# Kernel optimization log

Hardware: AMD Instinct MI355X
Metric: run time of the kernel (lower is better)

## Reference

```python
import jax, jax.numpy as jnp
import numpy as np
from jax.ops import segment_sum

N_NODES = 50000
N_EDGES = 800000
IN_DIM, HID_DIM, OUT_DIM = 128, 256, 128


def _glorot(key, shape):
    lim = np.sqrt(6.0 / (shape[0] + shape[1]))
    return jax.random.uniform(key, shape, jnp.float32, -lim, lim)


def setup_inputs() -> dict:
    key = jax.random.key(0)
    ks = jax.random.split(key, 4)
    x = jax.random.normal(ks[0], (N_NODES, IN_DIM), jnp.float32)
    edge_index = jax.random.randint(ks[1], (2, N_EDGES), 0, N_NODES, jnp.int64)
    W1 = _glorot(ks[2], (IN_DIM, HID_DIM))
    b1 = jnp.zeros((HID_DIM,), jnp.float32)
    W2 = _glorot(ks[3], (HID_DIM, OUT_DIM))
    b2 = jnp.zeros((OUT_DIM,), jnp.float32)
    return {"x": x, "edge_index": edge_index, "W1": W1, "b1": b1, "W2": W2, "b2": b2}


def gcn_conv(x, W, b, src, dst, n_nodes):
    # PyG GCNConv: x' = D^{-1/2} (A + I) D^{-1/2} (x W) + b
    h = x @ W  # [N, F_out]
    deg = segment_sum(jnp.ones_like(src, dtype=h.dtype), dst, num_segments=n_nodes) + 1.0  # +1 self loop
    dinv = jax.lax.rsqrt(deg)  # [N]
    norm = dinv[src] * dinv[dst]  # per-edge norm [E]
    msg = h[src] * norm[:, None]  # [E, F_out]
    agg = segment_sum(msg, dst, num_segments=n_nodes)
    agg = agg + h * (dinv * dinv)[:, None]  # self-loop term: norm_ii = dinv_i^2
    return agg + b


def reference(x, edge_index, W1, b1, W2, b2):
    src, dst = edge_index[0], edge_index[1]
    h = gcn_conv(x, W1, b1, src, dst, N_NODES)
    h = jax.nn.relu(h)
    out = gcn_conv(h, W2, b2, src, dst, N_NODES)
    return out
```

## Files before the change

kernel.cpp:

```cpp
#include <hip/hip_runtime.h>

#define N_NODES 50000
#define N_EDGES 800000
#define IN_DIM  128
#define HID_DIM 256
#define OUT_DIM 128
#define BUCKET_CAP 64
#define NCOARSE 196
#define CHUNK 4000
#define NBLK1 200
#define SEGCAP 64
#define HLD 264

typedef __attribute__((ext_vector_type(8))) short short8;
typedef __attribute__((ext_vector_type(4))) float f32x4;

__device__ inline ushort f2b(float f) {
    union { float f; unsigned u; } v; v.f = f;
    return (ushort)((v.u + 0x7FFFu + ((v.u >> 16) & 1u)) >> 16);
}
__device__ inline float b2f(ushort h) {
    union { unsigned u; float f; } v; v.u = ((unsigned)h) << 16;
    return v.f;
}
__device__ inline float2 u2f2(unsigned u) {
    float2 r; r.x = b2f((ushort)(u & 0xFFFFu)); r.y = b2f((ushort)(u >> 16)); return r;
}
__device__ inline unsigned f2u2(float a, float b) {
    return (unsigned)f2b(a) | ((unsigned)f2b(b) << 16);
}
__device__ inline void fma8(float2* acc, uint4 u, float n) {
    float2 v0 = u2f2(u.x), v1 = u2f2(u.y), v2 = u2f2(u.z), v3 = u2f2(u.w);
    acc[0].x += v0.x * n; acc[0].y += v0.y * n;
    acc[1].x += v1.x * n; acc[1].y += v1.y * n;
    acc[2].x += v2.x * n; acc[2].y += v2.y * n;
    acc[3].x += v3.x * n; acc[3].y += v3.y * n;
}


__global__ __launch_bounds__(256) void prep_kernel(const float* __restrict__ x,
                                                   const float* __restrict__ W1,
                                                   const float* __restrict__ W2,
                                                   const int* __restrict__ src,
                                                   const int* __restrict__ dst,
                                                   ushort* __restrict__ xb,
                                                   ushort* __restrict__ w1t,
                                                   ushort* __restrict__ w2t,
                                                   int* __restrict__ bcnt,
                                                   int* __restrict__ binbuf) {
    __shared__ int vals[CHUNK];
    __shared__ ushort lpos[CHUNK];
    __shared__ unsigned char lbin[CHUNK];
    __shared__ int hist[NCOARSE];
    const int b = blockIdx.x;
    const int t = threadIdx.x;
    if (b < 6250) {
        int i = b * 256 + t;
        float4 v = ((const float4*)x)[i];
        ushort4 o; o.x = f2b(v.x); o.y = f2b(v.y); o.z = f2b(v.z); o.w = f2b(v.w);
        ((ushort4*)xb)[i] = o;
    } else if (b < 6506) {
        int i = (b - 6250) * 256 + t;
        if (i < 32768) {
            int n = i >> 7, k = i & 127;
            w1t[i] = f2b(W1[k * HID_DIM + n]);
        } else {
            int j = i - 32768;
            int n = j >> 8, k = j & 255;
            w2t[j] = f2b(W2[k * OUT_DIM + n]);
        }
    } else {
        const int blk = b - 6506;
        const int e0 = blk * CHUNK;
        for (int i = t; i < NCOARSE; i += 256) hist[i] = 0;
        __syncthreads();
        for (int i = t; i < CHUNK; i += 256) {
            int s = src[e0 + i], d = dst[e0 + i];
            int bin = d >> 8;
            vals[i] = (s << 8) | (d & 255);
            lbin[i] = (unsigned char)bin;
            lpos[i] = (ushort)atomicAdd(&hist[bin], 1);
        }
        __syncthreads();
        for (int i = t; i < NCOARSE; i += 256) {
            int h = hist[i]; if (h > SEGCAP) h = SEGCAP;
            bcnt[i * NBLK1 + blk] = h;
        }
        for (int i = t; i < CHUNK; i += 256) {
            int bin = lbin[i];
            int p = lpos[i];
            if (p < SEGCAP) binbuf[((size_t)bin * NBLK1 + blk) * SEGCAP + p] = vals[i];
        }
    }
}


__global__ __launch_bounds__(256) void binpass2_kernel(const int* __restrict__ bcnt,
                                                       const int* __restrict__ binbuf,
                                                       int* __restrict__ cnt,
                                                       float* __restrict__ dinv,
                                                       int* __restrict__ bucket) {
    __shared__ int lcnt[256];
    __shared__ int lm[NBLK1];
    __shared__ int lbuck[256 * BUCKET_CAP];
    const int bin = blockIdx.x;
    const int t = threadIdx.x;
    lcnt[t] = 0;
    if (t < NBLK1) lm[t] = bcnt[bin * NBLK1 + t];
    __syncthreads();
    const int* bb = binbuf + (size_t)bin * NBLK1 * SEGCAP;
    for (int f = t; f < NBLK1 * SEGCAP; f += 256) {
        int blk = f >> 6;
        int sl = f & 63;
        if (sl < lm[blk]) {
            int v = bb[f];
            int dl = v & 255;
            int pos = atomicAdd(&lcnt[dl], 1);
            if (pos < BUCKET_CAP) lbuck[dl * BUCKET_CAP + pos] = v >> 8;
        }
    }
    __syncthreads();
    const int node0 = bin * 256;
    int node = node0 + t;
    if (node < N_NODES) {
        int c = lcnt[t] > BUCKET_CAP ? BUCKET_CAP : lcnt[t];
        cnt[node] = c;
        dinv[node] = rsqrtf((float)c + 1.0f);
    }
    int nvalid = N_NODES - node0; if (nvalid > 256) nvalid = 256;
    if (nvalid <= 0) return;
    int total4 = (nvalid * BUCKET_CAP) >> 2;
    int4* d4 = (int4*)(bucket + (size_t)node0 * BUCKET_CAP);
    const int4* s4 = (const int4*)lbuck;
    for (int j = t; j < total4; j += 256) d4[j] = s4[j];
}


__global__ __launch_bounds__(256) void gather0_kernel(const int* __restrict__ cnt,
                                                      const int* __restrict__ bucket,
                                                      const float* __restrict__ dinv,
                                                      const ushort* __restrict__ xb,
                                                      ushort* __restrict__ aggxb) {
    const int w = blockIdx.x * 4 + (threadIdx.x >> 6);
    const int lane = threadIdx.x & 63;
    const int grp = lane >> 4, sub = lane & 15;
    const int n = cnt[w];
    const float dd = dinv[w];
    int sv = 0; float nv = 0.f;
    if (lane < n) { sv = bucket[w * BUCKET_CAP + lane]; nv = dinv[sv] * dd; }

    float2 acc[4];
    if (grp == 0) {
        uint4 su = ((const uint4*)(xb + (size_t)w * IN_DIM))[sub];
        float sd = dd * dd;
        acc[0] = u2f2(su.x); acc[1] = u2f2(su.y); acc[2] = u2f2(su.z); acc[3] = u2f2(su.w);
#pragma unroll
        for (int j = 0; j < 4; ++j) { acc[j].x *= sd; acc[j].y *= sd; }
    } else {
#pragma unroll
        for (int j = 0; j < 4; ++j) acc[j] = {0.f, 0.f};
    }

    const int nr = (n + 15) & ~15;
    for (int i = 0; i < nr; i += 16) {
        int s0 = __shfl(sv, i + grp),      s1 = __shfl(sv, i + 4 + grp);
        int s2 = __shfl(sv, i + 8 + grp),  s3 = __shfl(sv, i + 12 + grp);
        float n0 = __shfl(nv, i + grp),     n1 = __shfl(nv, i + 4 + grp);
        float n2 = __shfl(nv, i + 8 + grp), n3 = __shfl(nv, i + 12 + grp);
        uint4 u0 = ((const uint4*)(xb + (size_t)s0 * IN_DIM))[sub];
        uint4 u1 = ((const uint4*)(xb + (size_t)s1 * IN_DIM))[sub];
        uint4 u2 = ((const uint4*)(xb + (size_t)s2 * IN_DIM))[sub];
        uint4 u3 = ((const uint4*)(xb + (size_t)s3 * IN_DIM))[sub];
        fma8(acc, u0, n0); fma8(acc, u1, n1); fma8(acc, u2, n2); fma8(acc, u3, n3);
    }
#pragma unroll
    for (int j = 0; j < 4; ++j) {
        acc[j].x += __shfl_down(acc[j].x, 32); acc[j].y += __shfl_down(acc[j].y, 32);
        acc[j].x += __shfl_down(acc[j].x, 16); acc[j].y += __shfl_down(acc[j].y, 16);
    }
    if (lane < 16) {
        uint4 o = {f2u2(acc[0].x, acc[0].y), f2u2(acc[1].x, acc[1].y),
                   f2u2(acc[2].x, acc[2].y), f2u2(acc[3].x, acc[3].y)};
        ((uint4*)(aggxb + (size_t)w * IN_DIM))[sub] = o;
    }
}


__global__ __launch_bounds__(256) void gemm12_mfma(const ushort* __restrict__ aggxb,
                                                   const ushort* __restrict__ w1t,
                                                   const float* __restrict__ b1,
                                                   const ushort* __restrict__ w2t,
                                                   ushort* __restrict__ h2b) {
    __shared__ ushort Hs[16 * HLD];
    const int row0 = blockIdx.x * 16;
    const int wv = threadIdx.x >> 6;
    const int lane = threadIdx.x & 63;
    const int l15 = lane & 15, q = lane >> 4;

    f32x4 acc1[4] = {{0.f, 0.f, 0.f, 0.f}, {0.f, 0.f, 0.f, 0.f},
                     {0.f, 0.f, 0.f, 0.f}, {0.f, 0.f, 0.f, 0.f}};
    const ushort* abase = aggxb + (size_t)(row0 + l15) * IN_DIM + q * 8;
#pragma unroll
    for (int kb = 0; kb < 4; ++kb) {
        short8 a = *(const short8*)(abase + kb * 32);
#pragma unroll
        for (int t = 0; t < 4; ++t) {
            int col = wv * 64 + t * 16 + l15;
            short8 bfr = *(const short8*)(w1t + (size_t)col * IN_DIM + kb * 32 + q * 8);
            acc1[t] = __builtin_amdgcn_mfma_f32_16x16x32_bf16(a, bfr, acc1[t], 0, 0, 0);
        }
    }
#pragma unroll
    for (int t = 0; t < 4; ++t) {
        int col = wv * 64 + t * 16 + l15;
        float bias = b1[col];
#pragma unroll
        for (int r = 0; r < 4; ++r) {
            int row = q * 4 + r;
            float v = acc1[t][r] + bias;
            Hs[row * HLD + col] = f2b(v > 0.f ? v : 0.f);
        }
    }
    __syncthreads();

    f32x4 acc2[2] = {{0.f, 0.f, 0.f, 0.f}, {0.f, 0.f, 0.f, 0.f}};
    const ushort* hbase = Hs + l15 * HLD + q * 8;
#pragma unroll
    for (int kb = 0; kb < 8; ++kb) {
        short8 a = *(const short8*)(hbase + kb * 32);
#pragma unroll
        for (int t = 0; t < 2; ++t) {
            int col = wv * 32 + t * 16 + l15;
            short8 bfr = *(const short8*)(w2t + (size_t)col * HID_DIM + kb * 32 + q * 8);
            acc2[t] = __builtin_amdgcn_mfma_f32_16x16x32_bf16(a, bfr, acc2[t], 0, 0, 0);
        }
    }
#pragma unroll
    for (int t = 0; t < 2; ++t) {
        int col = wv * 32 + t * 16 + l15;
#pragma unroll
        for (int r = 0; r < 4; ++r) {
            int row = row0 + q * 4 + r;
            h2b[(size_t)row * OUT_DIM + col] = f2b(acc2[t][r]);
        }
    }
}


__global__ __launch_bounds__(256) void gather2_kernel(const int* __restrict__ cnt,
                                                      const int* __restrict__ bucket,
                                                      const float* __restrict__ dinv,
                                                      const ushort* __restrict__ h2b,
                                                      const float* __restrict__ b2,
                                                      float* __restrict__ out) {
    const int w = blockIdx.x * 4 + (threadIdx.x >> 6);
    const int lane = threadIdx.x & 63;
    const int grp = lane >> 4, sub = lane & 15;
    const int n = cnt[w];
    const float dd = dinv[w];
    int sv = 0; float nv = 0.f;
    if (lane < n) { sv = bucket[w * BUCKET_CAP + lane]; nv = dinv[sv] * dd; }

    float2 acc[4];
    if (grp == 0) {
        uint4 su = ((const uint4*)(h2b + (size_t)w * OUT_DIM))[sub];
        float sd = dd * dd;
        acc[0] = u2f2(su.x); acc[1] = u2f2(su.y); acc[2] = u2f2(su.z); acc[3] = u2f2(su.w);
#pragma unroll
        for (int j = 0; j < 4; ++j) { acc[j].x *= sd; acc[j].y *= sd; }
    } else {
#pragma unroll
        for (int j = 0; j < 4; ++j) acc[j] = {0.f, 0.f};
    }

    const int nr = (n + 15) & ~15;
    for (int i = 0; i < nr; i += 16) {
        int s0 = __shfl(sv, i + grp),      s1 = __shfl(sv, i + 4 + grp);
        int s2 = __shfl(sv, i + 8 + grp),  s3 = __shfl(sv, i + 12 + grp);
        float n0 = __shfl(nv, i + grp),     n1 = __shfl(nv, i + 4 + grp);
        float n2 = __shfl(nv, i + 8 + grp), n3 = __shfl(nv, i + 12 + grp);
        uint4 u0 = ((const uint4*)(h2b + (size_t)s0 * OUT_DIM))[sub];
        uint4 u1 = ((const uint4*)(h2b + (size_t)s1 * OUT_DIM))[sub];
        uint4 u2 = ((const uint4*)(h2b + (size_t)s2 * OUT_DIM))[sub];
        uint4 u3 = ((const uint4*)(h2b + (size_t)s3 * OUT_DIM))[sub];
        fma8(acc, u0, n0); fma8(acc, u1, n1); fma8(acc, u2, n2); fma8(acc, u3, n3);
    }
#pragma unroll
    for (int j = 0; j < 4; ++j) {
        acc[j].x += __shfl_down(acc[j].x, 32); acc[j].y += __shfl_down(acc[j].y, 32);
        acc[j].x += __shfl_down(acc[j].x, 16); acc[j].y += __shfl_down(acc[j].y, 16);
    }
    if (lane < 16) {
        const float4* bp = (const float4*)b2;
        float4 b0 = bp[sub * 2], b1v = bp[sub * 2 + 1];
        float4 o0 = {acc[0].x + b0.x, acc[0].y + b0.y, acc[1].x + b0.z, acc[1].y + b0.w};
        float4 o1 = {acc[2].x + b1v.x, acc[2].y + b1v.y, acc[3].x + b1v.z, acc[3].y + b1v.w};
        float4* op = (float4*)(out + (size_t)w * OUT_DIM);
        op[sub * 2] = o0;
        op[sub * 2 + 1] = o1;
    }
}

extern "C" void kernel_launch(void* const* d_in, const int* in_sizes, int n_in,
                              void* d_out, int out_size, void* d_ws, size_t ws_size,
                              hipStream_t stream) {
    const float* x  = (const float*)d_in[0];
    const int*   ei = (const int*)d_in[1];
    const float* W1 = (const float*)d_in[2];
    const float* b1 = (const float*)d_in[3];
    const float* W2 = (const float*)d_in[4];
    const float* b2 = (const float*)d_in[5];
    float* out = (float*)d_out;

    const int* src = ei;
    const int* dst = ei + N_EDGES;

    char* ws = (char*)d_ws;
    int*    bcnt   = (int*)(ws);
    int*    cnt    = (int*)(ws + 160000);
    float*  dinv   = (float*)(ws + 360000);
    int*    bucket = (int*)(ws + 560000);
    int*    binbuf = (int*)(ws + 13360000);
    ushort* xb     = (ushort*)(ws + 23395200);
    ushort* w1t    = (ushort*)(ws + 36195200);
    ushort* w2t    = (ushort*)(ws + 36260736);
    ushort* aggxb  = (ushort*)(ws + 36326272);
    ushort* h2b    = (ushort*)(ws + 49126272);

    prep_kernel<<<6706, 256, 0, stream>>>(x, W1, W2, src, dst, xb, w1t, w2t, bcnt, binbuf);
    binpass2_kernel<<<NCOARSE, 256, 0, stream>>>(bcnt, binbuf, cnt, dinv, bucket);

    gather0_kernel<<<N_NODES / 4, 256, 0, stream>>>(cnt, bucket, dinv, xb, aggxb);
    gemm12_mfma<<<N_NODES / 16, 256, 0, stream>>>(aggxb, w1t, b1, w2t, h2b);

    gather2_kernel<<<N_NODES / 4, 256, 0, stream>>>(cnt, bucket, dinv, h2b, b2, out);
}
```

Before: 244.0 us.

## Process 64 rows per block in fused GEMM to reuse weight fragments

The fused two-layer MFMA GEMM now handles 64 rows per block instead of 16. Weight fragments for both GEMMs are loaded into registers once and reused across four 16-row sub-tiles, which cuts redundant global weight reads. Bounds clamping and guarded stores handle the partial last block. The cost is higher register and LDS use (launch_bounds 256,2), so occupancy drops and fewer blocks are launched.

Measured after the change: 215.5 us. -11.7%, faster.

```diff
diff --git a/kernel.cpp b/kernel.cpp
--- a/kernel.cpp
+++ b/kernel.cpp
@@ -11,6 +11,7 @@
 #define NBLK1 200
 #define SEGCAP 64
 #define HLD 264
+#define GROWS 64
 
 typedef __attribute__((ext_vector_type(8))) short short8;
 typedef __attribute__((ext_vector_type(4))) float f32x4;
@@ -186,64 +187,91 @@
 }
 
 
-__global__ __launch_bounds__(256) void gemm12_mfma(const ushort* __restrict__ aggxb,
-                                                   const ushort* __restrict__ w1t,
-                                                   const float* __restrict__ b1,
-                                                   const ushort* __restrict__ w2t,
-                                                   ushort* __restrict__ h2b) {
-    __shared__ ushort Hs[16 * HLD];
-    const int row0 = blockIdx.x * 16;
+__global__ __launch_bounds__(256, 2) void gemm12_mfma(const ushort* __restrict__ aggxb,
+                                                      const ushort* __restrict__ w1t,
+                                                      const float* __restrict__ b1,
+                                                      const ushort* __restrict__ w2t,
+                                                      ushort* __restrict__ h2b) {
+    __shared__ ushort Hs[GROWS * HLD];
+    const int row0 = blockIdx.x * GROWS;
     const int wv = threadIdx.x >> 6;
     const int lane = threadIdx.x & 63;
     const int l15 = lane & 15, q = lane >> 4;
 
-    f32x4 acc1[4] = {{0.f, 0.f, 0.f, 0.f}, {0.f, 0.f, 0.f, 0.f},
-                     {0.f, 0.f, 0.f, 0.f}, {0.f, 0.f, 0.f, 0.f}};
-    const ushort* abase = aggxb + (size_t)(row0 + l15) * IN_DIM + q * 8;
-#pragma unroll
-    for (int kb = 0; kb < 4; ++kb) {
-        short8 a = *(const short8*)(abase + kb * 32);
+    short8 bf1[16];
+#pragma unroll
+    for (int kb = 0; kb < 4; ++kb)
 #pragma unroll
         for (int t = 0; t < 4; ++t) {
             int col = wv * 64 + t * 16 + l15;
-            short8 bfr = *(const short8*)(w1t + (size_t)col * IN_DIM + kb * 32 + q * 8);
-            acc1[t] = __builtin_amdgcn_mfma_f32_16x16x32_bf16(a, bfr, acc1[t], 0, 0, 0);
-        }
-    }
+            bf1[kb * 4 + t] = *(const short8*)(w1t + (size_t)col * IN_DIM + kb * 32 + q * 8);
+        }
+    short8 af[4][4];
+#pragma unroll
+    for (int sub = 0; sub < 4; ++sub) {
+        int ar = row0 + sub * 16 + l15;
+        if (ar >= N_NODES) ar = N_NODES - 1;
+        const ushort* ab = aggxb + (size_t)ar * IN_DIM + q * 8;
+#pragma unroll
+        for (int kb = 0; kb < 4; ++kb) af[sub][kb] = *(const short8*)(ab + kb * 32);
+    }
+    f32x4 acc1[4][4] = {};
+#pragma unroll
+    for (int sub = 0; sub < 4; ++sub)
+#pragma unroll
+        for (int kb = 0; kb < 4; ++kb)
+#pragma unroll
+            for (int t = 0; t < 4; ++t)
+                acc1[sub][t] = __builtin_amdgcn_mfma_f32_16x16x32_bf16(
+                    af[sub][kb], bf1[kb * 4 + t], acc1[sub][t], 0, 0, 0);
 #pragma unroll
     for (int t = 0; t < 4; ++t) {
         int col = wv * 64 + t * 16 + l15;
         float bias = b1[col];
 #pragma unroll
-        for (int r = 0; r < 4; ++r) {
-            int row = q * 4 + r;
-            float v = acc1[t][r] + bias;
-            Hs[row * HLD + col] = f2b(v > 0.f ? v : 0.f);
-        }
+        for (int sub = 0; sub < 4; ++sub)
+#pragma unroll
+            for (int r = 0; r < 4; ++r) {
+                int row = sub * 16 + q * 4 + r;
+                float v = acc1[sub][t][r] + bias;
+                Hs[row * HLD + col] = f2b(v > 0.f ? v : 0.f);
+            }
     }
     __syncthreads();
 
-    f32x4 acc2[2] = {{0.f, 0.f, 0.f, 0.f}, {0.f, 0.f, 0.f, 0.f}};
-    const ushort* hbase = Hs + l15 * HLD + q * 8;
-#pragma unroll
-    for (int kb = 0; kb < 8; ++kb) {
-        short8 a = *(const short8*)(hbase + kb * 32);
+    short8 bf2[16];
+#pragma unroll
+    for (int kb = 0; kb < 8; ++kb)
 #pragma unroll
         for (int t = 0; t < 2; ++t) {
             int col = wv * 32 + t * 16 + l15;
-            short8 bfr = *(const short8*)(w2t + (size_t)col * HID_DIM + kb * 32 + q * 8);
-            acc2[t] = __builtin_amdgcn_mfma_f32_16x16x32_bf16(a, bfr, acc2[t], 0, 0, 0);
-        }
-    }
-#pragma unroll
-    for (int t = 0; t < 2; ++t) {
-        int col = wv * 32 + t * 16 + l15;
-#pragma unroll
-        for (int r = 0; r < 4; ++r) {
-            int row = row0 + q * 4 + r;
-            h2b[(size_t)row * OUT_DIM + col] = f2b(acc2[t][r]);
-        }
-    }
+            bf2[kb * 2 + t] = *(const short8*)(w2t + (size_t)col * HID_DIM + kb * 32 + q * 8);
+        }
+    f32x4 acc2[4][2] = {};
+#pragma unroll
+    for (int sub = 0; sub < 4; ++sub) {
+        const ushort* hb = Hs + (sub * 16 + l15) * HLD + q * 8;
+#pragma unroll
+        for (int kb = 0; kb < 8; ++kb) {
+            short8 a = *(const short8*)(hb + kb * 32);
+#pragma unroll
+            for (int t = 0; t < 2; ++t)
+                acc2[sub][t] = __builtin_amdgcn_mfma_f32_16x16x32_bf16(
+                    a, bf2[kb * 2 + t], acc2[sub][t], 0, 0, 0);
+        }
+    }
+#pragma unroll
+    for (int sub = 0; sub < 4; ++sub)
+#pragma unroll
+        for (int t = 0; t < 2; ++t) {
+            int col = wv * 32 + t * 16 + l15;
+#pragma unroll
+            for (int r = 0; r < 4; ++r) {
+                int row = row0 + sub * 16 + q * 4 + r;
+                if (row < N_NODES)
+                    h2b[(size_t)row * OUT_DIM + col] = f2b(acc2[sub][t][r]);
+            }
+        }
 }
 
 
@@ -331,7 +359,7 @@
     binpass2_kernel<<<NCOARSE, 256, 0, stream>>>(bcnt, binbuf, cnt, dinv, bucket);
 
     gather0_kernel<<<N_NODES / 4, 256, 0, stream>>>(cnt, bucket, dinv, xb, aggxb);
-    gemm12_mfma<<<N_NODES / 16, 256, 0, stream>>>(aggxb, w1t, b1, w2t, h2b);
+    gemm12_mfma<<<(N_NODES + GROWS - 1) / GROWS, 256, 0, stream>>>(aggxb, w1t, b1, w2t, h2b);
 
     gather2_kernel<<<N_NODES / 4, 256, 0, stream>>>(cnt, bucket, dinv, h2b, b2, out);
 }
```
